# Optimization experiments

Measured on AMD Instinct MI355X. Metric: run time of the kernel, lower is better.

The kernel has to match this reference:

```python
import jax, jax.numpy as jnp
import numpy as np

N, D = 8192, 512
K = 32          # k_neighbors (k = min(k_neighbors, n-1))
N_PAIRS = 2048  # n_samples


def setup_inputs() -> dict:
    key = jax.random.key(0)
    k1, k2, k3 = jax.random.split(key, 3)
    embeddings = jax.random.normal(k1, (N, D), dtype=jnp.float32)
    reference_second_order = jax.random.uniform(k2, (N_PAIRS, K), dtype=jnp.float32)
    # stands in for torch.randperm(n)[:n_pairs]
    pair_indices = jax.random.randint(k3, (N_PAIRS,), 0, N, dtype=jnp.int64)
    return {
        "embeddings": embeddings,
        "reference_second_order": reference_second_order,
        "pair_indices": pair_indices,
    }


def _second_order(embeddings, pair_indices):
    n = embeddings.shape[0]
    k = K
    # pairwise euclidean distances (cdist p=2)
    sq = jnp.sum(embeddings * embeddings, axis=1)
    d2 = sq[:, None] + sq[None, :] - 2.0 * (embeddings @ embeddings.T)
    dists = jnp.sqrt(jnp.maximum(d2, 0.0))
    # k+1 smallest, drop self
    _, idx = jax.lax.top_k(-dists, k + 1)
    knn = idx[:, 1:]  # [n, k]
    # one-hot neighborhood membership: M[i, j] = 1 iff j in N_i
    M = jnp.zeros((n, n), dtype=embeddings.dtype)
    M = M.at[jnp.arange(n)[:, None], knn].set(1.0)
    # |N_i cap N_j| for sampled rows i against ALL j via one matmul
    Mp = M[pair_indices]          # [P, n]
    G = Mp @ M.T                  # [P, n]  intersection counts
    nb = knn[pair_indices]        # [P, k]  the j's we actually need
    overlap = jnp.take_along_axis(G, nb, axis=1) / k  # [P, k]
    return jnp.sort(overlap, axis=1)


def reference(embeddings, reference_second_order, pair_indices):
    curr = _second_order(embeddings, pair_indices)  # [P, k]
    # shapes already match reference (n=P, k=K) so [:n,:k] slice is identity
    loss = jnp.mean((curr - reference_second_order) ** 2)
    return loss
```

## Files before the change

### kernel.cpp

```cpp
#include <hip/hip_runtime.h>
#include <hip/hip_bf16.h>

#define NROWS 8192
#define DIM   512
#define KNN   32
#define NPAIR 2048

#define STRIPS 4
#define SCOLS  2048
#define CHUNK  256
#define BK     32
#define MROWS  64
#define NSTEP  ((SCOLS / CHUNK) * (DIM / BK))

typedef __attribute__((ext_vector_type(8)))  short bf16x8;
typedef __attribute__((ext_vector_type(16))) float f32x16;

__device__ __forceinline__ void gload16(const void* g, void* l) {
    __builtin_amdgcn_global_load_lds(
        (const __attribute__((address_space(1))) void*)g,
        (__attribute__((address_space(3))) void*)l, 16, 0, 0);
}

__device__ __forceinline__ unsigned short bfrne(float x) {
    unsigned u = __float_as_uint(x);
    return (unsigned short)((u + 0x7FFFu + ((u >> 16) & 1u)) >> 16);
}

__global__ __launch_bounds__(256) void sqnorm_k(const float* __restrict__ E,
                                                float* __restrict__ sq) {
    int row  = blockIdx.x * 4 + (threadIdx.x >> 6);
    int lane = threadIdx.x & 63;
    const float4* e4 = reinterpret_cast<const float4*>(E + (size_t)row * DIM);
    float acc = 0.f;
#pragma unroll
    for (int t = 0; t < 2; ++t) {
        float4 v = e4[lane + 64 * t];
        acc += v.x * v.x + v.y * v.y + v.z * v.z + v.w * v.w;
    }
#pragma unroll
    for (int off = 32; off; off >>= 1) acc += __shfl_xor(acc, off);
    if (lane == 0) sq[row] = acc;
}

__global__ __launch_bounds__(256) void prep_k(const float* __restrict__ E,
                                              short* __restrict__ Phi,
                                              short* __restrict__ Plo) {
    const int p    = blockIdx.x * 256 + threadIdx.x;
    const int lane = p & 63;
    const int s    = (p >> 6) & 31;
    const int rb   = p >> 11;
    const int row  = rb * 32 + (lane & 31);
    const int k0   = s * 16 + (lane >> 5) * 8;
    const float4* src = reinterpret_cast<const float4*>(E + (size_t)row * DIM + k0);
    float4 x0 = src[0], x1 = src[1];
    float xs[8] = {x0.x, x0.y, x0.z, x0.w, x1.x, x1.y, x1.z, x1.w};
    short hs[8], ls[8];
#pragma unroll
    for (int e = 0; e < 8; ++e) {
        unsigned short hb = bfrne(xs[e]);
        float hf = __uint_as_float(((unsigned)hb) << 16);
        hs[e] = (short)hb;
        ls[e] = (short)bfrne(xs[e] - hf);
    }
    bf16x8 h, l;
#pragma unroll
    for (int e = 0; e < 8; ++e) { h[e] = hs[e]; l[e] = ls[e]; }
    *reinterpret_cast<bf16x8*>(Phi + (size_t)p * 8) = h;
    *reinterpret_cast<bf16x8*>(Plo + (size_t)p * 8) = l;
}

__global__ __launch_bounds__(512, 4) void distsel_k(const short* __restrict__ Phi,
                                                    const short* __restrict__ Plo,
                                                    const float* __restrict__ sq,
                                                    float* __restrict__ cval,
                                                    int* __restrict__ cidx) {
    extern __shared__ char smem[];
    short* At = (short*)smem;
    short* Bt = (short*)(smem + 8192);
    float* SC = (float*)(smem + 40960);

    const int tid  = threadIdx.x;
    const int w    = tid >> 6;
    const int lane = tid & 63;
    const int kh   = lane >> 5;
    const int c32  = lane & 31;
    const int rbk  = blockIdx.x >> 2;
    const int st   = blockIdx.x & 3;
    const int r0   = rbk * MROWS;
    const int cstrip = st * SCOLS;
    const float INF_F = __builtin_inff();

    const int rb  = w >> 2;
    const int cb0 = 2 * (w & 3);

    auto stage = [&](int t) {
        const int ch = t >> 4, ksg = t & 15;
        {
            const int m = w >> 2, rbL = (w >> 1) & 1, s = w & 1;
            const short* Pm = m ? Plo : Phi;
            const size_t pk = ((size_t)(((r0 >> 5) + rbL) * 32 + 2 * ksg + s) * 64 + lane) * 8;
            gload16(Pm + pk, At + (((m * 2 + rbL) * 2 + s) * 512));
        }
#pragma unroll
        for (int j = 0; j < 4; ++j) {
            const int q = 4 * w + j;
            const int m = q >> 4, cbL = (q >> 1) & 7, s = q & 1;
            const short* Pm = m ? Plo : Phi;
            const size_t pk = ((size_t)(((cstrip >> 5) + ch * 8 + cbL) * 32 + 2 * ksg + s) * 64 + lane) * 8;
            gload16(Pm + pk, Bt + (((m * 8 + cbL) * 2 + s) * 512));
        }
    };

    float Tv[8]; int Ti[8];
#pragma unroll
    for (int r = 0; r < 8; ++r) { Tv[r] = INF_F; Ti[r] = -1; }

    f32x16 acc[2];
#pragma unroll
    for (int ci = 0; ci < 2; ++ci)
#pragma unroll
        for (int m = 0; m < 16; ++m) acc[ci][m] = 0.f;

    for (int t = 0; t < NSTEP; ++t) {
        stage(t);
        __syncthreads();

#pragma unroll
        for (int s = 0; s < 2; ++s) {
            const bf16x8 ah = *(const bf16x8*)(At + (((0 * 2 + rb) * 2 + s) * 512) + lane * 8);
            const bf16x8 al = *(const bf16x8*)(At + (((1 * 2 + rb) * 2 + s) * 512) + lane * 8);
#pragma unroll
            for (int ci = 0; ci < 2; ++ci) {
                const bf16x8 bh = *(const bf16x8*)(Bt + (((0 * 8 + cb0 + ci) * 2 + s) * 512) + lane * 8);
                const bf16x8 bl = *(const bf16x8*)(Bt + (((1 * 8 + cb0 + ci) * 2 + s) * 512) + lane * 8);
                acc[ci] = __builtin_amdgcn_mfma_f32_32x32x16_bf16(ah, bh, acc[ci], 0, 0, 0);
                acc[ci] = __builtin_amdgcn_mfma_f32_32x32x16_bf16(ah, bl, acc[ci], 0, 0, 0);
                acc[ci] = __builtin_amdgcn_mfma_f32_32x32x16_bf16(al, bh, acc[ci], 0, 0, 0);
            }
        }

        if ((t & 15) != 15) {
            __syncthreads();
        } else {
            const int ch = t >> 4;
            const int c0 = cstrip + ch * CHUNK;
            const float sqv0 = sq[c0 + (cb0 + 0) * 32 + c32];
            const float sqv1 = sq[c0 + (cb0 + 1) * 32 + c32];
#pragma unroll
            for (int ph = 0; ph < 2; ++ph) {
                if (rb == ph) {
#pragma unroll
                    for (int ci = 0; ci < 2; ++ci) {
                        const float sv = ci ? sqv1 : sqv0;
#pragma unroll
                        for (int m = 0; m < 16; ++m) {
                            const int sub = (m & 3) + 8 * (m >> 2) + 4 * kh;
                            SC[sub * CHUNK + (cb0 + ci) * 32 + c32] = sv - 2.f * acc[ci][m];
                        }
                    }
                }
                __syncthreads();
#pragma unroll
                for (int rr = 0; rr < 4; ++rr) {
                    float& tv = Tv[ph * 4 + rr];
                    int&   ti = Ti[ph * 4 + rr];
                    const float4 f = *(const float4*)(SC + (4 * w + rr) * CHUNK + 4 * lane);
                    float mn = fminf(fminf(f.x, f.y), fminf(f.z, f.w));
                    float t0e = INF_F;
                    if (ch == 0) {
                        float v = mn;
#pragma unroll
                        for (int k = 2; k <= 64; k <<= 1)
#pragma unroll
                            for (int j = k >> 1; j; j >>= 1) {
                                float o = __shfl_xor(v, j);
                                const bool lower = ((lane & j) == 0);
                                const bool dir   = ((lane & k) == 0);
                                v = (lower == dir) ? fminf(v, o) : fmaxf(v, o);
                            }
                        float t0 = __shfl(v, 32);
                        t0e = t0 + fabsf(t0) * 1e-6f + 1e-30f;
                    }
                    float lthr = __shfl(tv, 32);
                    float gate = fminf(lthr, t0e);
                    while (true) {
                        unsigned long long bal = __ballot(mn < gate);
                        if (!bal) break;
                        const int src = (int)__builtin_ctzll(bal);
                        const float gx = __shfl(f.x, src);
                        const float gy = __shfl(f.y, src);
                        const float gz = __shfl(f.z, src);
                        const float gw = __shfl(f.w, src);
                        const int jc0 = c0 + 4 * src;
                        if (lane == src) mn = INF_F;
#define INS(VV, JJ)                                                         \
                        if ((VV) < gate) {                                  \
                            float pv = __shfl_up(tv, 1);                    \
                            int   pi = __shfl_up(ti, 1);                    \
                            if (lane == 0) pv = -INF_F;                     \
                            if (tv > (VV)) {                                \
                                const bool tk = pv > (VV);                  \
                                tv = tk ? pv : (VV);                        \
                                ti = tk ? pi : (JJ);                        \
                            }                                               \
                            lthr = __shfl(tv, 32);                          \
                            gate = fminf(lthr, t0e);                        \
                        }
                        INS(gx, jc0); INS(gy, jc0 + 1); INS(gz, jc0 + 2); INS(gw, jc0 + 3);
#undef INS
                    }
                }
                __syncthreads();
            }
#pragma unroll
            for (int ci = 0; ci < 2; ++ci)
#pragma unroll
                for (int m = 0; m < 16; ++m) acc[ci][m] = 0.f;
        }
    }

#pragma unroll
    for (int ph = 0; ph < 2; ++ph)
#pragma unroll
        for (int rr = 0; rr < 4; ++rr) {
            const int grow = r0 + 32 * ph + 4 * w + rr;
            if (lane <= 32) {
                cval[(size_t)grow * (STRIPS * 33) + st * 33 + lane] = Tv[ph * 4 + rr];
                cidx[(size_t)grow * (STRIPS * 33) + st * 33 + lane] = Ti[ph * 4 + rr];
            }
        }
}

__global__ __launch_bounds__(256) void merge_k(const float* __restrict__ cval,
                                               const int* __restrict__ cidx,
                                               int* __restrict__ knn) {
    const int row  = blockIdx.x * 4 + (threadIdx.x >> 6);
    const int lane = threadIdx.x & 63;
    const float INF_F = __builtin_inff();
    const float* cv = cval + (size_t)row * (STRIPS * 33);
    const int*   ci = cidx + (size_t)row * (STRIPS * 33);
    float v0 = cv[lane];       int i0 = ci[lane];
    float v1 = cv[lane + 64];  int i1 = ci[lane + 64];
    float v2 = (lane + 128 < STRIPS * 33) ? cv[lane + 128] : INF_F;
    int   i2 = (lane + 128 < STRIPS * 33) ? ci[lane + 128] : 0x7FFFFFFF;
    for (int it = 0; it < 33; ++it) {
        float mv = v0; int mi = i0; int ms = 0;
        if (v1 < mv || (v1 == mv && i1 < mi)) { mv = v1; mi = i1; ms = 1; }
        if (v2 < mv || (v2 == mv && i2 < mi)) { mv = v2; mi = i2; ms = 2; }
        float bv = mv; int bi = mi; int bl = lane;
#pragma unroll
        for (int off = 32; off; off >>= 1) {
            float ov = __shfl_xor(bv, off);
            int   oi = __shfl_xor(bi, off);
            int   ol = __shfl_xor(bl, off);
            if (ov < bv || (ov == bv && oi < bi)) { bv = ov; bi = oi; bl = ol; }
        }
        if (it > 0 && lane == 0) knn[(size_t)row * KNN + it - 1] = bi;
        if (lane == bl) {
            if (ms == 0) v0 = INF_F; else if (ms == 1) v1 = INF_F; else v2 = INF_F;
        }
    }
}

__global__ __launch_bounds__(64) void overlap_k(const int* __restrict__ knn,
                                                const int* __restrict__ pairs,
                                                const float* __restrict__ refso,
                                                float* __restrict__ partial) {
    const int p    = blockIdx.x;
    const int lane = threadIdx.x;
    __shared__ int si[KNN];
    const int i = pairs[p];
    if (lane < KNN) si[lane] = knn[(size_t)i * KNN + lane];
    __syncthreads();

    float v = 0.f;
    if (lane < KNN) {
        const int j = si[lane];
        int t[KNN];
        const int4* kj = reinterpret_cast<const int4*>(knn + (size_t)j * KNN);
#pragma unroll
        for (int b = 0; b < KNN / 4; ++b) {
            int4 q = kj[b];
            t[4 * b + 0] = q.x; t[4 * b + 1] = q.y;
            t[4 * b + 2] = q.z; t[4 * b + 3] = q.w;
        }
        int cnt = 0;
        for (int a = 0; a < KNN; ++a) {
            int sa = si[a];
#pragma unroll
            for (int b = 0; b < KNN; ++b) cnt += (t[b] == sa);
        }
        v = (float)cnt * (1.0f / KNN);
    }
    int rank = 0;
    for (int q = 0; q < KNN; ++q) {
        float ov = __shfl(v, q);
        rank += (lane < KNN) && ((ov < v) || (ov == v && q < lane));
    }
    float err = 0.f;
    if (lane < KNN) {
        float r = refso[(size_t)p * KNN + rank];
        float d = v - r;
        err = d * d;
    }
#pragma unroll
    for (int off = 32; off; off >>= 1) err += __shfl_xor(err, off);
    if (lane == 0) partial[p] = err;
}

__global__ __launch_bounds__(256) void final_k(const float* __restrict__ partial,
                                               float* __restrict__ out) {
    const int tid = threadIdx.x;
    float a = 0.f;
    for (int q = tid; q < NPAIR; q += 256) a += partial[q];
#pragma unroll
    for (int off = 32; off; off >>= 1) a += __shfl_xor(a, off);
    __shared__ float red[4];
    if ((tid & 63) == 0) red[tid >> 6] = a;
    __syncthreads();
    if (tid == 0)
        out[0] = (red[0] + red[1] + red[2] + red[3]) * (1.0f / (NPAIR * KNN));
}

__global__ __launch_bounds__(256) void dist_topk_k(const float* __restrict__ E,
                                                   const float* __restrict__ sq,
                                                   int* __restrict__ knn) {
    extern __shared__ float sc[];
    const int tid = threadIdx.x;
    const int r0  = blockIdx.x * 4;
    const float4* a0 = reinterpret_cast<const float4*>(E + (size_t)(r0 + 0) * DIM);
    const float4* a1 = reinterpret_cast<const float4*>(E + (size_t)(r0 + 1) * DIM);
    const float4* a2 = reinterpret_cast<const float4*>(E + (size_t)(r0 + 2) * DIM);
    const float4* a3 = reinterpret_cast<const float4*>(E + (size_t)(r0 + 3) * DIM);
    for (int tile = 0; tile < NROWS / 256; ++tile) {
        int j = tile * 256 + tid;
        const float4* bj = reinterpret_cast<const float4*>(E + (size_t)j * DIM);
        float acc0 = 0.f, acc1 = 0.f, acc2 = 0.f, acc3 = 0.f;
#pragma unroll 4
        for (int dd = 0; dd < DIM / 4; ++dd) {
            float4 b  = bj[dd];
            float4 x0 = a0[dd], x1 = a1[dd], x2 = a2[dd], x3 = a3[dd];
            acc0 += x0.x * b.x + x0.y * b.y + x0.z * b.z + x0.w * b.w;
            acc1 += x1.x * b.x + x1.y * b.y + x1.z * b.z + x1.w * b.w;
            acc2 += x2.x * b.x + x2.y * b.y + x2.z * b.z + x2.w * b.w;
            acc3 += x3.x * b.x + x3.y * b.y + x3.z * b.z + x3.w * b.w;
        }
        float sj = sq[j];
        sc[0 * NROWS + j] = sj - 2.f * acc0;
        sc[1 * NROWS + j] = sj - 2.f * acc1;
        sc[2 * NROWS + j] = sj - 2.f * acc2;
        sc[3 * NROWS + j] = sj - 2.f * acc3;
    }
    __syncthreads();
    const int w    = tid >> 6;
    const int lane = tid & 63;
    float* s = sc + w * NROWS;
    const float INF = __builtin_inff();
    float m[4]; int mi[4];
#pragma unroll
    for (int b = 0; b < 4; ++b) {
        float bm = INF; int bmi = NROWS;
        for (int t = 0; t < 32; ++t) {
            int j = lane + 64 * (b * 32 + t);
            float v = s[j];
            if (v < bm || (v == bm && j < bmi)) { bm = v; bmi = j; }
        }
        m[b] = bm; mi[b] = bmi;
    }
    const int row = r0 + w;
    for (int it = 0; it < KNN + 1; ++it) {
        float cvv = m[0]; int cii = mi[0];
#pragma unroll
        for (int b = 1; b < 4; ++b)
            if (m[b] < cvv || (m[b] == cvv && mi[b] < cii)) { cvv = m[b]; cii = mi[b]; }
        float bv = cvv; int bi = cii;
#pragma unroll
        for (int off = 32; off; off >>= 1) {
            float ov = __shfl_xor(bv, off);
            int   oi = __shfl_xor(bi, off);
            if (ov < bv || (ov == bv && oi < bi)) { bv = ov; bi = oi; }
        }
        if (it > 0 && lane == 0) knn[(size_t)row * KNN + (it - 1)] = bi;
        int ol = bi & 63;
        if (lane == ol) {
            s[bi] = INF;
            int b = (bi >> 6) >> 5;
            float bm = INF; int bmi = NROWS;
            for (int t = 0; t < 32; ++t) {
                int j = lane + 64 * (b * 32 + t);
                float v = s[j];
                if (v < bm || (v == bm && j < bmi)) { bm = v; bmi = j; }
            }
            m[b] = bm; mi[b] = bmi;
        }
    }
}

extern "C" void kernel_launch(void* const* d_in, const int* in_sizes, int n_in,
                              void* d_out, int out_size, void* d_ws, size_t ws_size,
                              hipStream_t stream) {
    const float* E     = (const float*)d_in[0];
    const float* refso = (const float*)d_in[1];
    const int*   pairs = (const int*)d_in[2];
    float* out = (float*)d_out;

    char* ws = (char*)d_ws;
    float* sq      = (float*)ws;
    float* partial = (float*)(ws + 32768);
    int*   knn     = (int*)(ws + 40960);
    short* Phi     = (short*)(ws + 1089536);
    short* Plo     = (short*)(ws + 9478144);
    float* cval    = (float*)(ws + 17866752);
    int*   cidx    = (int*)(ws + 22192128);
    const size_t NEED = 26517504;

    if (ws_size >= NEED) {
        hipFuncSetAttribute((const void*)distsel_k,
                            hipFuncAttributeMaxDynamicSharedMemorySize, 73728);
        sqnorm_k<<<NROWS / 4, 256, 0, stream>>>(E, sq);
        prep_k<<<NROWS * DIM / 8 / 256, 256, 0, stream>>>(E, Phi, Plo);
        distsel_k<<<(NROWS / MROWS) * STRIPS, 512, 73728, stream>>>(Phi, Plo, sq, cval, cidx);
        merge_k<<<NROWS / 4, 256, 0, stream>>>(cval, cidx, knn);
    } else {
        hipFuncSetAttribute((const void*)dist_topk_k,
                            hipFuncAttributeMaxDynamicSharedMemorySize, 131072);
        sqnorm_k<<<NROWS / 4, 256, 0, stream>>>(E, sq);
        dist_topk_k<<<NROWS / 4, 256, 131072, stream>>>(E, sq, knn);
    }
    overlap_k<<<NPAIR, 64, 0, stream>>>(knn, pairs, refso, partial);
    final_k<<<1, 256, 0, stream>>>(partial, out);
}
```

Baseline: 571.4 us.

## Split distance-select into eight column strips with smaller smem for occupancy

Doubles the number of column strips so twice as many blocks run the fused distance-GEMM plus top-k selection, each covering half as many columns. The score staging buffer is shrunk to one row per wave per phase, and the occupancy hint is raised to allow more resident blocks. The candidate buffers become strip-major, and the merge kernel now reduces 264 candidates per row instead of 132. The cost is more selection passes and barriers per block, more candidate traffic, and a longer merge.

```diff
diff --git a/kernel.cpp b/kernel.cpp
--- a/kernel.cpp
+++ b/kernel.cpp
@@ -6,12 +6,13 @@
 #define KNN   32
 #define NPAIR 2048
 
-#define STRIPS 4
-#define SCOLS  2048
+#define STRIPS 8
+#define SCOLS  1024
 #define CHUNK  256
 #define BK     32
 #define MROWS  64
 #define NSTEP  ((SCOLS / CHUNK) * (DIM / BK))
+#define NCAND  (STRIPS * 33)
 
 typedef __attribute__((ext_vector_type(8)))  short bf16x8;
 typedef __attribute__((ext_vector_type(16))) float f32x16;
@@ -70,7 +71,7 @@
     *reinterpret_cast<bf16x8*>(Plo + (size_t)p * 8) = l;
 }
 
-__global__ __launch_bounds__(512, 4) void distsel_k(const short* __restrict__ Phi,
+__global__ __launch_bounds__(512, 6) void distsel_k(const short* __restrict__ Phi,
                                                     const short* __restrict__ Plo,
                                                     const float* __restrict__ sq,
                                                     float* __restrict__ cval,
@@ -85,8 +86,8 @@
     const int lane = tid & 63;
     const int kh   = lane >> 5;
     const int c32  = lane & 31;
-    const int rbk  = blockIdx.x >> 2;
-    const int st   = blockIdx.x & 3;
+    const int rbk  = blockIdx.x >> 3;
+    const int st   = blockIdx.x & 7;
     const int r0   = rbk * MROWS;
     const int cstrip = st * SCOLS;
     const float INF_F = __builtin_inff();
@@ -148,24 +149,25 @@
             const float sqv0 = sq[c0 + (cb0 + 0) * 32 + c32];
             const float sqv1 = sq[c0 + (cb0 + 1) * 32 + c32];
 #pragma unroll
-            for (int ph = 0; ph < 2; ++ph) {
-                if (rb == ph) {
+            for (int q = 0; q < 8; ++q) {
+                if (rb == (q >> 2)) {
+                    const int j = q & 3;
 #pragma unroll
                     for (int ci = 0; ci < 2; ++ci) {
                         const float sv = ci ? sqv1 : sqv0;
 #pragma unroll
-                        for (int m = 0; m < 16; ++m) {
-                            const int sub = (m & 3) + 8 * (m >> 2) + 4 * kh;
-                            SC[sub * CHUNK + (cb0 + ci) * 32 + c32] = sv - 2.f * acc[ci][m];
+                        for (int mm = 0; mm < 4; ++mm) {
+                            const int m = 4 * j + mm;
+                            SC[(mm + 4 * kh) * CHUNK + (cb0 + ci) * 32 + c32] =
+                                sv - 2.f * acc[ci][m];
                         }
                     }
                 }
                 __syncthreads();
-#pragma unroll
-                for (int rr = 0; rr < 4; ++rr) {
-                    float& tv = Tv[ph * 4 + rr];
-                    int&   ti = Ti[ph * 4 + rr];
-                    const float4 f = *(const float4*)(SC + (4 * w + rr) * CHUNK + 4 * lane);
+                {
+                    float& tv = Tv[q];
+                    int&   ti = Ti[q];
+                    const float4 f = *(const float4*)(SC + w * CHUNK + 4 * lane);
                     float mn = fminf(fminf(f.x, f.y), fminf(f.z, f.w));
                     float t0e = INF_F;
                     if (ch == 0) {
@@ -173,9 +175,9 @@
 #pragma unroll
                         for (int k = 2; k <= 64; k <<= 1)
 #pragma unroll
-                            for (int j = k >> 1; j; j >>= 1) {
-                                float o = __shfl_xor(v, j);
-                                const bool lower = ((lane & j) == 0);
+                            for (int jj = k >> 1; jj; jj >>= 1) {
+                                float o = __shfl_xor(v, jj);
+                                const bool lower = ((lane & jj) == 0);
                                 const bool dir   = ((lane & k) == 0);
                                 v = (lower == dir) ? fminf(v, o) : fmaxf(v, o);
                             }
@@ -221,15 +223,13 @@
     }
 
 #pragma unroll
-    for (int ph = 0; ph < 2; ++ph)
-#pragma unroll
-        for (int rr = 0; rr < 4; ++rr) {
-            const int grow = r0 + 32 * ph + 4 * w + rr;
-            if (lane <= 32) {
-                cval[(size_t)grow * (STRIPS * 33) + st * 33 + lane] = Tv[ph * 4 + rr];
-                cidx[(size_t)grow * (STRIPS * 33) + st * 33 + lane] = Ti[ph * 4 + rr];
-            }
-        }
+    for (int q = 0; q < 8; ++q) {
+        const int grow = r0 + 32 * (q >> 2) + 8 * (q & 3) + w;
+        if (lane <= 32) {
+            cval[(size_t)st * (NROWS * 33) + (size_t)grow * 33 + lane] = Tv[q];
+            cidx[(size_t)st * (NROWS * 33) + (size_t)grow * 33 + lane] = Ti[q];
+        }
+    }
 }
 
 __global__ __launch_bounds__(256) void merge_k(const float* __restrict__ cval,
@@ -238,16 +238,22 @@
     const int row  = blockIdx.x * 4 + (threadIdx.x >> 6);
     const int lane = threadIdx.x & 63;
     const float INF_F = __builtin_inff();
-    const float* cv = cval + (size_t)row * (STRIPS * 33);
-    const int*   ci = cidx + (size_t)row * (STRIPS * 33);
-    float v0 = cv[lane];       int i0 = ci[lane];
-    float v1 = cv[lane + 64];  int i1 = ci[lane + 64];
-    float v2 = (lane + 128 < STRIPS * 33) ? cv[lane + 128] : INF_F;
-    int   i2 = (lane + 128 < STRIPS * 33) ? ci[lane + 128] : 0x7FFFFFFF;
+    float vv[5]; int ii[5];
+#pragma unroll
+    for (int k = 0; k < 5; ++k) {
+        const int idx = lane + 64 * k;
+        const bool ok = idx < NCAND;
+        const int stt = idx / 33;
+        const int e   = idx - 33 * stt;
+        const size_t off = (size_t)stt * (NROWS * 33) + (size_t)row * 33 + e;
+        vv[k] = ok ? cval[off] : INF_F;
+        ii[k] = ok ? cidx[off] : 0x7FFFFFFF;
+    }
     for (int it = 0; it < 33; ++it) {
-        float mv = v0; int mi = i0; int ms = 0;
-        if (v1 < mv || (v1 == mv && i1 < mi)) { mv = v1; mi = i1; ms = 1; }
-        if (v2 < mv || (v2 == mv && i2 < mi)) { mv = v2; mi = i2; ms = 2; }
+        float mv = vv[0]; int mi = ii[0]; int ms = 0;
+#pragma unroll
+        for (int k = 1; k < 5; ++k)
+            if (vv[k] < mv || (vv[k] == mv && ii[k] < mi)) { mv = vv[k]; mi = ii[k]; ms = k; }
         float bv = mv; int bi = mi; int bl = lane;
 #pragma unroll
         for (int off = 32; off; off >>= 1) {
@@ -258,7 +264,9 @@
         }
         if (it > 0 && lane == 0) knn[(size_t)row * KNN + it - 1] = bi;
         if (lane == bl) {
-            if (ms == 0) v0 = INF_F; else if (ms == 1) v1 = INF_F; else v2 = INF_F;
+#pragma unroll
+            for (int k = 0; k < 5; ++k)
+                if (k == ms) vv[k] = INF_F;
         }
     }
 }
@@ -412,15 +420,15 @@
     short* Phi     = (short*)(ws + 1089536);
     short* Plo     = (short*)(ws + 9478144);
     float* cval    = (float*)(ws + 17866752);
-    int*   cidx    = (int*)(ws + 22192128);
-    const size_t NEED = 26517504;
+    int*   cidx    = (int*)(ws + 26517504);
+    const size_t NEED = 35168256;
 
     if (ws_size >= NEED) {
         hipFuncSetAttribute((const void*)distsel_k,
-                            hipFuncAttributeMaxDynamicSharedMemorySize, 73728);
+                            hipFuncAttributeMaxDynamicSharedMemorySize, 49152);
         sqnorm_k<<<NROWS / 4, 256, 0, stream>>>(E, sq);
         prep_k<<<NROWS * DIM / 8 / 256, 256, 0, stream>>>(E, Phi, Plo);
-        distsel_k<<<(NROWS / MROWS) * STRIPS, 512, 73728, stream>>>(Phi, Plo, sq, cval, cidx);
+        distsel_k<<<(NROWS / MROWS) * STRIPS, 512, 49152, stream>>>(Phi, Plo, sq, cval, cidx);
         merge_k<<<NROWS / 4, 256, 0, stream>>>(cval, cidx, knn);
     } else {
         hipFuncSetAttribute((const void*)dist_topk_k,
```

Result: slower. 803.7 us (+40.6%).
